# Performance work log

Hardware: AMD Instinct MI355X
Metric: run time of the kernel (lower is better)

The kernel has to match this reference:

```python
import jax, jax.numpy as jnp
import numpy as np

N_STREAMS = 4
SINKHORN_ITERS = 20
EPS = 1e-8


def sinkhorn_knopp(log_mat, num_iters=SINKHORN_ITERS, eps=EPS):
    mat = jnp.exp(log_mat)
    def body(_, m):
        m = m / (m.sum(axis=-2, keepdims=True) + eps)
        m = m / (m.sum(axis=-1, keepdims=True) + eps)
        return m
    return jax.lax.fori_loop(0, num_iters, body, mat)


def setup_inputs() -> dict:
    key = jax.random.key(0)
    B, L, C = 4, 2048, 1024
    n = N_STREAMS
    hidden = 4 * C
    ks = jax.random.split(key, 8)
    def xavier(k, shape):
        fan_in, fan_out = shape[0], shape[1]
        lim = np.sqrt(6.0 / (fan_in + fan_out))
        return jax.random.uniform(k, shape, jnp.float32, -lim, lim)
    return {
        "x": jax.random.normal(ks[0], (B, L, C), jnp.float32),
        "rms_weight": jnp.ones((C * n,), jnp.float32),
        "W_dyn": xavier(ks[1], (C * n, n * n + 2 * n)),  # Linear no-bias, stored [in,out]
        "bias_pre": jnp.zeros((1, n), jnp.float32),
        "bias_post": jnp.zeros((1, n), jnp.float32),
        "bias_res": jnp.zeros((n, n), jnp.float32),
        "alpha_pre": jnp.full((1,), 0.01, jnp.float32),
        "alpha_post": jnp.full((1,), 0.01, jnp.float32),
        "alpha_res": jnp.full((1,), 0.01, jnp.float32),
        "W1": xavier(ks[2], (C, hidden)),
        "b1": jnp.zeros((hidden,), jnp.float32),
        "W2": xavier(ks[3], (hidden, C)),
        "b2": jnp.zeros((C,), jnp.float32),
        "Wout": xavier(ks[4], (C * n, C)),
        "bout": jnp.zeros((C,), jnp.float32),
    }


def reference(x, rms_weight, W_dyn, bias_pre, bias_post, bias_res,
              alpha_pre, alpha_post, alpha_res, W1, b1, W2, b2, Wout, bout):
    B, L, C = x.shape
    n = bias_pre.shape[1]
    # x expanded across streams (broadcast view, no copy)
    x_exp = jnp.broadcast_to(x[:, :, None, :], (B, L, n, C))  # [B,L,n,C]
    x_flat = x_exp.reshape(B, L, n * C)
    # RMSNorm
    rms = jnp.sqrt(jnp.mean(x_flat * x_flat, axis=-1, keepdims=True) + EPS)
    x_norm = x_flat / rms * rms_weight
    # dynamic projection
    dynamic = x_norm @ W_dyn  # [B,L,n*n+2n]
    dyn_pre = dynamic[..., :n]
    dyn_post = dynamic[..., n:2 * n]
    dyn_res = dynamic[..., 2 * n:].reshape(B, L, n, n)
    H_pre = jax.nn.sigmoid(alpha_pre * dyn_pre + bias_pre)            # [B,L,n]
    H_post = 2.0 * jax.nn.sigmoid(alpha_post * dyn_post + bias_post)  # [B,L,n]
    H_res = sinkhorn_knopp(alpha_res * dyn_res + bias_res)            # [B,L,n,n]
    # pre-mix streams then residual MLP
    pre_mixed = jnp.einsum('bln,blnc->blc', H_pre, x_exp)
    h = jax.nn.gelu(pre_mixed @ W1 + b1, approximate=False)
    f_out = h @ W2 + b2  # [B,L,C]
    # post mixing + doubly-stochastic residual mixing
    post_mixed = H_post[..., None] * f_out[:, :, None, :]             # [B,L,n,C]
    res_mixed = jnp.einsum('blnm,blmc->blnc', H_res, x_exp)
    merged = (res_mixed + post_mixed).reshape(B, L, n * C)
    return merged @ Wout + bout + x
```

## Files before the change

### kernel.cpp

```cpp
#include <hip/hip_runtime.h>

typedef unsigned short u16;
typedef __bf16 bf16x8 __attribute__((ext_vector_type(8)));
typedef float f32x4 __attribute__((ext_vector_type(4)));

__device__ __forceinline__ u16 f2bf(float f) {
  unsigned int u = __builtin_bit_cast(unsigned int, f);
  u += 0x7fffu + ((u >> 16) & 1u);
  return (u16)(u >> 16);
}

__device__ __forceinline__ void gload_lds16(const u16* g, u16* l) {
  __builtin_amdgcn_global_load_lds((const __attribute__((address_space(1))) unsigned int*)g,
                                   (__attribute__((address_space(3))) unsigned int*)l,
                                   16, 0, 0);
}

__device__ __forceinline__ float gelu_erf(float v) {
  const float z = v * 0.70710678118654752f;
  const float az = fabsf(z);
  const float t = __builtin_amdgcn_rcpf(1.0f + 0.3275911f * az);
  const float p = t * (0.254829592f +
                  t * (-0.284496736f +
                  t * (1.421413741f +
                  t * (-1.453152027f + t * 1.061405429f))));
  const float e = __expf(-az * az);
  float er = 1.0f - p * e;
  er = (z < 0.f) ? -er : er;
  return 0.5f * v * (1.0f + er);
}


__global__ __launch_bounds__(256) void weff_kernel(const float* __restrict__ rmsw,
                                                   const float* __restrict__ Wdyn,
                                                   float* __restrict__ WT) {
  int idx = blockIdx.x * 256 + threadIdx.x;
  int j = idx >> 10, c = idx & 1023;
  float s = 0.f;
#pragma unroll
  for (int st = 0; st < 4; ++st) {
    int r = st * 1024 + c;
    s += rmsw[r] * Wdyn[(long)r * 24 + j];
  }
  WT[idx] = s;
}

__global__ __launch_bounds__(256) void pack_all(const float* __restrict__ W1,
                                                const float* __restrict__ W2,
                                                const float* __restrict__ WO,
                                                u16* __restrict__ F1,
                                                u16* __restrict__ F2,
                                                u16* __restrict__ FO) {
  const int blk = blockIdx.x;
  const int sel = blk >> 11;
  const float* W;
  u16* FMB;
  int lgN, KC;
  if (sel == 0)      { W = W1; FMB = F1; lgN = 12; KC = 32; }
  else if (sel == 1) { W = W2; FMB = F2; lgN = 10; KC = 128; }
  else               { W = WO; FMB = FO; lgN = 10; KC = 128; }
  const long gid = (long)(blk & 2047) * 256 + threadIdx.x;
  const int N = 1 << lgN;
  const int n = (int)(gid & (N - 1));
  const int k0 = (int)(gid >> lgN) * 8;
  unsigned int p[4];
#pragma unroll
  for (int d = 0; d < 4; ++d) {
    const float lo = W[(long)(k0 + 2 * d) * N + n];
    const float hi = W[(long)(k0 + 2 * d + 1) * N + n];
    p[d] = (unsigned)f2bf(lo) | ((unsigned)f2bf(hi) << 16);
  }
  const long ad = ((long)(n >> 4) * KC + (k0 >> 5)) * 512 +
                  ((n & 15) + (((k0 >> 3) & 3) << 4)) * 8;
  *(uint4*)(FMB + ad) = make_uint4(p[0], p[1], p[2], p[3]);
}

__global__ __launch_bounds__(512) void prep_tokens(
    const float* __restrict__ x, const float* __restrict__ WT,
    const float* __restrict__ bias_pre, const float* __restrict__ bias_post,
    const float* __restrict__ bias_res, const float* __restrict__ a_pre,
    const float* __restrict__ a_post, const float* __restrict__ a_res,
    u16* __restrict__ preA, float* __restrict__ scal) {
  const int tid = threadIdx.x;
  const int b = blockIdx.x;
  const long t0 = (long)b * 16;

  __shared__ float red[32][16][26];
  __shared__ float tot2[16][26];
  __shared__ float spre[16];

  {
    const int tt = tid & 15;
    const int cc = tid >> 4;
    const float* xp = x + (t0 + tt) * 1024 + cc * 32;
    float part[25];
#pragma unroll
    for (int j = 0; j < 25; ++j) part[j] = 0.f;
#pragma unroll
    for (int g = 0; g < 8; ++g) {
      const float4 xv = *(const float4*)(xp + g * 4);
      part[24] += xv.x * xv.x + xv.y * xv.y + xv.z * xv.z + xv.w * xv.w;
#pragma unroll
      for (int j = 0; j < 24; ++j) {
        const float4 wv = *(const float4*)(WT + (long)j * 1024 + cc * 32 + g * 4);
        part[j] += xv.x * wv.x + xv.y * wv.y + xv.z * wv.z + xv.w * wv.w;
      }
    }
#pragma unroll
    for (int j = 0; j < 25; ++j) red[cc][tt][j] = part[j];
  }
  __syncthreads();

  {
    const int tt = tid >> 5;
    const int j = tid & 31;
    if (j < 25) {
      float s = 0.f;
#pragma unroll
      for (int cc = 0; cc < 32; ++cc) s += red[cc][tt][j];
      tot2[tt][j] = s;
    }
  }
  __syncthreads();

  if (tid < 256) {
    const int tt = tid >> 4;
    const int m = tid & 15;
    const long t = t0 + tt;
    const float rms = sqrtf(tot2[tt][24] * (1.0f / 1024.0f) + 1e-8f);
    const float rinv = 1.0f / rms;

    if (m == 0) {
      const float ap = a_pre[0];
      float s_pre = 0.f;
#pragma unroll
      for (int i = 0; i < 4; ++i)
        s_pre += 1.f / (1.f + expf(-(ap * tot2[tt][i] * rinv + bias_pre[i])));
      spre[tt] = s_pre;
    }
    if (m < 4) {
      const float apo = a_post[0];
      float hp = 2.f / (1.f + expf(-(apo * tot2[tt][4 + m] * rinv + bias_post[m])));
      scal[t * 8 + 4 + m] = hp;
    }
    const float ar = a_res[0];
    float Mv = expf(ar * tot2[tt][8 + m] * rinv + bias_res[m]);
#pragma unroll
    for (int it = 0; it < 20; ++it) {
      float cs = Mv + __shfl_xor(Mv, 4);
      cs += __shfl_xor(cs, 8);
      Mv = Mv / (cs + 1e-8f);
      float rs = Mv + __shfl_xor(Mv, 1);
      rs += __shfl_xor(rs, 2);
      Mv = Mv / (rs + 1e-8f);
    }
    float rs = Mv + __shfl_xor(Mv, 1);
    rs += __shfl_xor(rs, 2);
    if ((m & 3) == 0) scal[t * 8 + (m >> 2)] = rs;
  }
  __syncthreads();

  {
    const int w = tid >> 6;
    const int lane = tid & 63;
    const int tl = lane & 15;
    const int co = (lane >> 4) * 8;
    const float sp = spre[tl];
#pragma unroll
    for (int p = 0; p < 4; ++p) {
      const int ki = p * 8 + w;
      const float* xr = x + (t0 + tl) * 1024 + ki * 32 + co;
      const float4 xa = *(const float4*)(xr);
      const float4 xb = *(const float4*)(xr + 4);
      unsigned q0 = (unsigned)f2bf(sp * xa.x) | ((unsigned)f2bf(sp * xa.y) << 16);
      unsigned q1 = (unsigned)f2bf(sp * xa.z) | ((unsigned)f2bf(sp * xa.w) << 16);
      unsigned q2 = (unsigned)f2bf(sp * xb.x) | ((unsigned)f2bf(sp * xb.y) << 16);
      unsigned q3 = (unsigned)f2bf(sp * xb.z) | ((unsigned)f2bf(sp * xb.w) << 16);
      *(uint4*)(preA + ((long)b * 32 + ki) * 512 + lane * 8) = make_uint4(q0, q1, q2, q3);
    }
  }
}

template <int EPI>
__global__ __launch_bounds__(256, 4) void gemm_fm(const u16* __restrict__ A,
                                                  const u16* __restrict__ B,
                                                  const int KCtot, const int GX,
                                                  const int N, const int KCout,
                                                  const float* __restrict__ bias,
                                                  const float* __restrict__ X,
                                                  const float* __restrict__ scal,
                                                  void* __restrict__ dstv) {
  const int tid = threadIdx.x;
  const int lane = tid & 63;
  const int wave = tid >> 6;
  const int wm = wave >> 1, wn = wave & 1;
  const int b = blockIdx.x;
  const int c = b & 7;
  const int s = b >> 3;
  const int bx = s % GX;
  const int by = c * 8 + s / GX;

  __shared__ u16 lds[2][16][512];

  const u16* gb[4];
  u16* lc[4];
#pragma unroll
  for (int l = 0; l < 4; ++l) {
    const int t = wave * 4 + l;
    gb[l] = (t < 8) ? (A + (long)(by * 8 + t) * KCtot * 512 + lane * 8)
                    : (B + (long)(bx * 8 + (t - 8)) * KCtot * 512 + lane * 8);
    lc[l] = &lds[0][t][0];
  }

#define STAGE(buf, kt)                                             \
  {                                                                \
    const long ko = (long)(kt)*512;                                \
    _Pragma("unroll") for (int l = 0; l < 4; ++l)                  \
        gload_lds16(gb[l] + ko, lc[l] + (buf)*8192);               \
  }

  f32x4 acc[4][4] = {};

  STAGE(0, 0);
  __syncthreads();

  for (int kt = 0; kt < KCtot; ++kt) {
    const int cur = kt & 1;
    if (kt + 1 < KCtot) STAGE(cur ^ 1, kt + 1);
    bf16x8 af[4], bfr[4];
#pragma unroll
    for (int i = 0; i < 4; ++i) {
      af[i] = *(const bf16x8*)&lds[cur][wm * 4 + i][lane * 8];
      bfr[i] = *(const bf16x8*)&lds[cur][8 + wn * 4 + i][lane * 8];
    }
#pragma unroll
    for (int i = 0; i < 4; ++i)
#pragma unroll
      for (int j = 0; j < 4; ++j)
        acc[i][j] = __builtin_amdgcn_mfma_f32_16x16x32_bf16(af[i], bfr[j], acc[i][j], 0, 0, 0);
    __syncthreads();
  }
#undef STAGE

  u16* ep = ((u16*)lds) + wave * 4096;

  if constexpr (EPI == 0) {
    u16* dst = (u16*)dstv;
#pragma unroll
    for (int i = 0; i < 4; ++i)
#pragma unroll
      for (int j = 0; j < 4; ++j) {
        const int col = bx * 128 + wn * 64 + j * 16 + (lane & 15);
        const float bcol = bias[col];
#pragma unroll
        for (int r = 0; r < 4; ++r) {
          const float g = gelu_erf(acc[i][j][r] + bcol);
          const int lp = ((lane >> 4) * 4 + r) | ((((j & 1) << 1) | ((lane & 15) >> 3)) << 4);
          ep[(i * 2 + (j >> 1)) * 512 + lp * 8 + (lane & 7)] = f2bf(g);
        }
      }
    __syncthreads();
#pragma unroll
    for (int ch = 0; ch < 8; ++ch) {
      const int i = ch >> 1, jc = ch & 1;
      const long row16 = by * 8 + wm * 4 + i;
      const long col32 = bx * 4 + wn * 2 + jc;
      *(uint4*)(dst + (row16 * KCout + col32) * 512 + lane * 8) =
          *(const uint4*)(ep + ch * 512 + lane * 8);
    }
  } else if constexpr (EPI == 1) {
    u16* dst = (u16*)dstv;
#pragma unroll
    for (int i = 0; i < 4; ++i) {
      float rr[4][4], hh[4][4];
#pragma unroll
      for (int r = 0; r < 4; ++r) {
        const int row = by * 128 + wm * 64 + i * 16 + (lane >> 4) * 4 + r;
        const float4 rv = *(const float4*)(scal + (long)row * 8);
        const float4 hv = *(const float4*)(scal + (long)row * 8 + 4);
        rr[r][0] = rv.x; rr[r][1] = rv.y; rr[r][2] = rv.z; rr[r][3] = rv.w;
        hh[r][0] = hv.x; hh[r][1] = hv.y; hh[r][2] = hv.z; hh[r][3] = hv.w;
      }
#pragma unroll
      for (int jc = 0; jc < 2; ++jc) {
        __syncthreads();
#pragma unroll
        for (int jj = 0; jj < 2; ++jj) {
          const int j = jc * 2 + jj;
          const int col = bx * 128 + wn * 64 + j * 16 + (lane & 15);
          const float bcol = bias[col];
#pragma unroll
          for (int r = 0; r < 4; ++r) {
            const int row = by * 128 + wm * 64 + i * 16 + (lane >> 4) * 4 + r;
            const float f = acc[i][j][r] + bcol;
            const float xval = X[(long)row * 1024 + col];
            const int lp = ((lane >> 4) * 4 + r) | (((jj << 1) | ((lane & 15) >> 3)) << 4);
#pragma unroll
            for (int ss = 0; ss < 4; ++ss)
              ep[ss * 512 + lp * 8 + (lane & 7)] = f2bf(rr[r][ss] * xval + hh[r][ss] * f);
          }
        }
        __syncthreads();
        const long row16 = by * 8 + wm * 4 + i;
        const long col32 = bx * 4 + wn * 2 + jc;
#pragma unroll
        for (int ss = 0; ss < 4; ++ss)
          *(uint4*)(dst + (row16 * 128 + (long)ss * 32 + col32) * 512 + lane * 8) =
              *(const uint4*)(ep + ss * 512 + lane * 8);
      }
    }
  } else {
    float* dst = (float*)dstv;
    float* ep32 = (float*)ep;
#pragma unroll
    for (int half = 0; half < 2; ++half) {
      __syncthreads();
#pragma unroll
      for (int i2 = 0; i2 < 2; ++i2) {
        const int i = half * 2 + i2;
#pragma unroll
        for (int j = 0; j < 4; ++j) {
          const int col = bx * 128 + wn * 64 + j * 16 + (lane & 15);
          const float bcol = bias[col];
#pragma unroll
          for (int r = 0; r < 4; ++r) {
            const long row = by * 128 + wm * 64 + i * 16 + (lane >> 4) * 4 + r;
            ep32[(i2 * 16 + (lane >> 4) * 4 + r) * 64 + j * 16 + (lane & 15)] =
                acc[i][j][r] + bcol + X[row * 1024 + col];
          }
        }
      }
      __syncthreads();
#pragma unroll
      for (int q = 0; q < 8; ++q) {
        const int lr = q * 4 + (lane >> 4);
        const long row = by * 128 + wm * 64 + half * 32 + lr;
        const long col = bx * 128 + wn * 64 + (lane & 15) * 4;
        *(float4*)(dst + row * 1024 + col) =
            *(const float4*)(ep32 + lr * 64 + (lane & 15) * 4);
      }
    }
  }
}

extern "C" void kernel_launch(void* const* d_in, const int* in_sizes, int n_in,
                              void* d_out, int out_size, void* d_ws, size_t ws_size,
                              hipStream_t stream) {
  (void)in_sizes; (void)n_in; (void)out_size; (void)ws_size;
  const float* x = (const float*)d_in[0];
  const float* rmsw = (const float*)d_in[1];
  const float* Wdyn = (const float*)d_in[2];
  const float* bias_pre = (const float*)d_in[3];
  const float* bias_post = (const float*)d_in[4];
  const float* bias_res = (const float*)d_in[5];
  const float* a_pre = (const float*)d_in[6];
  const float* a_post = (const float*)d_in[7];
  const float* a_res = (const float*)d_in[8];
  const float* W1 = (const float*)d_in[9];
  const float* b1 = (const float*)d_in[10];
  const float* W2 = (const float*)d_in[11];
  const float* b2 = (const float*)d_in[12];
  const float* Wout = (const float*)d_in[13];
  const float* bout = (const float*)d_in[14];
  float* out = (float*)d_out;
  char* ws = (char*)d_ws;

  constexpr size_t MB = 1048576;
  u16* W1fm = (u16*)(ws);
  u16* W2fm = (u16*)(ws + 8 * MB);
  u16* WOfm = (u16*)(ws + 16 * MB);
  float* WT = (float*)(ws + 24 * MB);
  float* scal = (float*)(ws + 24 * MB + 98304);
  u16* h = (u16*)(ws + 25 * MB);
  u16* merged = (u16*)(ws + 89 * MB);
  u16* preA = (u16*)(ws + 89 * MB);

  weff_kernel<<<96, 256, 0, stream>>>(rmsw, Wdyn, WT);
  pack_all<<<6144, 256, 0, stream>>>(W1, W2, Wout, W1fm, W2fm, WOfm);
  prep_tokens<<<512, 512, 0, stream>>>(x, WT, bias_pre, bias_post, bias_res,
                                       a_pre, a_post, a_res, preA, scal);
  gemm_fm<0><<<2048, 256, 0, stream>>>(preA, W1fm, 32, 32, 4096, 128, b1, nullptr, nullptr, h);
  gemm_fm<1><<<512, 256, 0, stream>>>(h, W2fm, 128, 8, 1024, 128, b2, x, scal, merged);
  gemm_fm<2><<<512, 256, 0, stream>>>(merged, WOfm, 128, 8, 1024, 0, bout, x, nullptr, out);
}
```

Baseline: 431.1 us.

## Enlarge GEMM tiles to 512 threads with 4-stage LDS pipeline and manual waitcnts

```diff
diff --git a/kernel.cpp b/kernel.cpp
--- a/kernel.cpp
+++ b/kernel.cpp
@@ -181,76 +181,94 @@
   }
 }
 
-template <int EPI>
-__global__ __launch_bounds__(256, 4) void gemm_fm(const u16* __restrict__ A,
-                                                  const u16* __restrict__ B,
-                                                  const int KCtot, const int GX,
-                                                  const int N, const int KCout,
-                                                  const float* __restrict__ bias,
-                                                  const float* __restrict__ X,
-                                                  const float* __restrict__ scal,
-                                                  void* __restrict__ dstv) {
+template <int EPI, int NT, int LGGX>
+__global__ __launch_bounds__(512, 2) void gemm_fm2(const u16* __restrict__ A,
+                                                   const u16* __restrict__ B,
+                                                   const int KCtot, const int KCout,
+                                                   const float* __restrict__ bias,
+                                                   const float* __restrict__ X,
+                                                   const float* __restrict__ scal,
+                                                   void* __restrict__ dstv) {
+  constexpr int CH = 16 + NT;
+  constexpr int SC = CH / 8;
+  constexpr int AI = (NT == 16) ? 8 : 4;
   const int tid = threadIdx.x;
   const int lane = tid & 63;
   const int wave = tid >> 6;
-  const int wm = wave >> 1, wn = wave & 1;
+  const int wm = (NT == 16) ? (wave >> 2) : (wave >> 1);
+  const int wn = (NT == 16) ? (wave & 3) : (wave & 1);
   const int b = blockIdx.x;
   const int c = b & 7;
   const int s = b >> 3;
-  const int bx = s % GX;
-  const int by = c * 8 + s / GX;
-
-  __shared__ u16 lds[2][16][512];
+  const int bx = s & ((1 << LGGX) - 1);
+  const int by = c * 4 + (s >> LGGX);
+
+  __shared__ u16 lds[4][CH][512];
+  u16* const l0 = (u16*)lds;
 
   const u16* gb[4];
-  u16* lc[4];
-#pragma unroll
-  for (int l = 0; l < 4; ++l) {
-    const int t = wave * 4 + l;
-    gb[l] = (t < 8) ? (A + (long)(by * 8 + t) * KCtot * 512 + lane * 8)
-                    : (B + (long)(bx * 8 + (t - 8)) * KCtot * 512 + lane * 8);
-    lc[l] = &lds[0][t][0];
-  }
-
-#define STAGE(buf, kt)                                             \
-  {                                                                \
-    const long ko = (long)(kt)*512;                                \
-    _Pragma("unroll") for (int l = 0; l < 4; ++l)                  \
-        gload_lds16(gb[l] + ko, lc[l] + (buf)*8192);               \
-  }
-
-  f32x4 acc[4][4] = {};
-
-  STAGE(0, 0);
-  __syncthreads();
+#pragma unroll
+  for (int l = 0; l < SC; ++l) {
+    const int t = wave * SC + l;
+    gb[l] = (t < 16) ? (A + ((long)(by * 16 + t) * KCtot) * 512 + lane * 8)
+                     : (B + ((long)(bx * NT + (t - 16)) * KCtot) * 512 + lane * 8);
+  }
+
+#define STG(kt)                                                              \
+  {                                                                          \
+    u16* cb_ = l0 + (((kt) & 3) * CH + wave * SC) * 512;                     \
+    const long ko_ = (long)(kt)*512;                                         \
+    _Pragma("unroll") for (int l_ = 0; l_ < SC; ++l_)                        \
+        gload_lds16(gb[l_] + ko_, cb_ + l_ * 512);                           \
+  }
+
+  f32x4 acc[AI][4] = {};
+
+  STG(0); STG(1); STG(2);
+  if constexpr (SC == 4) asm volatile("s_waitcnt vmcnt(8)" ::: "memory");
+  else                   asm volatile("s_waitcnt vmcnt(6)" ::: "memory");
+  __builtin_amdgcn_s_barrier();
 
   for (int kt = 0; kt < KCtot; ++kt) {
-    const int cur = kt & 1;
-    if (kt + 1 < KCtot) STAGE(cur ^ 1, kt + 1);
-    bf16x8 af[4], bfr[4];
-#pragma unroll
-    for (int i = 0; i < 4; ++i) {
-      af[i] = *(const bf16x8*)&lds[cur][wm * 4 + i][lane * 8];
-      bfr[i] = *(const bf16x8*)&lds[cur][8 + wn * 4 + i][lane * 8];
-    }
-#pragma unroll
-    for (int i = 0; i < 4; ++i)
+    if (kt + 3 < KCtot) STG(kt + 3);
+    const u16* cb = l0 + (kt & 3) * (CH * 512);
+    bf16x8 af[AI], bf[4];
+#pragma unroll
+    for (int i = 0; i < AI; ++i)
+      af[i] = *(const bf16x8*)(cb + (wm * AI + i) * 512 + lane * 8);
+#pragma unroll
+    for (int j = 0; j < 4; ++j)
+      bf[j] = *(const bf16x8*)(cb + (16 + wn * 4 + j) * 512 + lane * 8);
+    asm volatile("s_waitcnt lgkmcnt(0)" ::: "memory");
+    __builtin_amdgcn_sched_barrier(0);
+    __builtin_amdgcn_s_setprio(1);
+#pragma unroll
+    for (int i = 0; i < AI; ++i)
 #pragma unroll
       for (int j = 0; j < 4; ++j)
-        acc[i][j] = __builtin_amdgcn_mfma_f32_16x16x32_bf16(af[i], bfr[j], acc[i][j], 0, 0, 0);
-    __syncthreads();
-  }
-#undef STAGE
-
-  u16* ep = ((u16*)lds) + wave * 4096;
+        acc[i][j] = __builtin_amdgcn_mfma_f32_16x16x32_bf16(af[i], bf[j], acc[i][j], 0, 0, 0);
+    __builtin_amdgcn_s_setprio(0);
+    if (kt + 4 <= KCtot) {
+      if constexpr (SC == 4) asm volatile("s_waitcnt vmcnt(8)" ::: "memory");
+      else                   asm volatile("s_waitcnt vmcnt(6)" ::: "memory");
+    } else if (kt + 3 == KCtot) {
+      if constexpr (SC == 4) asm volatile("s_waitcnt vmcnt(4)" ::: "memory");
+      else                   asm volatile("s_waitcnt vmcnt(3)" ::: "memory");
+    } else {
+      asm volatile("s_waitcnt vmcnt(0)" ::: "memory");
+    }
+    __builtin_amdgcn_s_barrier();
+  }
+#undef STG
 
   if constexpr (EPI == 0) {
     u16* dst = (u16*)dstv;
-#pragma unroll
-    for (int i = 0; i < 4; ++i)
+    u16* ep = l0 + wave * 8192;
+#pragma unroll
+    for (int i = 0; i < AI; ++i)
 #pragma unroll
       for (int j = 0; j < 4; ++j) {
-        const int col = bx * 128 + wn * 64 + j * 16 + (lane & 15);
+        const int col = bx * 256 + wn * 64 + j * 16 + (lane & 15);
         const float bcol = bias[col];
 #pragma unroll
         for (int r = 0; r < 4; ++r) {
@@ -259,23 +277,23 @@
           ep[(i * 2 + (j >> 1)) * 512 + lp * 8 + (lane & 7)] = f2bf(g);
         }
       }
-    __syncthreads();
-#pragma unroll
-    for (int ch = 0; ch < 8; ++ch) {
+#pragma unroll
+    for (int ch = 0; ch < 2 * AI; ++ch) {
       const int i = ch >> 1, jc = ch & 1;
-      const long row16 = by * 8 + wm * 4 + i;
-      const long col32 = bx * 4 + wn * 2 + jc;
+      const long row16 = by * 16 + wm * 8 + i;
+      const long col32 = bx * 8 + wn * 2 + jc;
       *(uint4*)(dst + (row16 * KCout + col32) * 512 + lane * 8) =
           *(const uint4*)(ep + ch * 512 + lane * 8);
     }
   } else if constexpr (EPI == 1) {
     u16* dst = (u16*)dstv;
-#pragma unroll
-    for (int i = 0; i < 4; ++i) {
+    u16* ep = l0 + wave * 4096;
+#pragma unroll
+    for (int i = 0; i < AI; ++i) {
       float rr[4][4], hh[4][4];
 #pragma unroll
       for (int r = 0; r < 4; ++r) {
-        const int row = by * 128 + wm * 64 + i * 16 + (lane >> 4) * 4 + r;
+        const int row = by * 256 + wm * 64 + i * 16 + (lane >> 4) * 4 + r;
         const float4 rv = *(const float4*)(scal + (long)row * 8);
         const float4 hv = *(const float4*)(scal + (long)row * 8 + 4);
         rr[r][0] = rv.x; rr[r][1] = rv.y; rr[r][2] = rv.z; rr[r][3] = rv.w;
@@ -283,7 +301,6 @@
       }
 #pragma unroll
       for (int jc = 0; jc < 2; ++jc) {
-        __syncthreads();
 #pragma unroll
         for (int jj = 0; jj < 2; ++jj) {
           const int j = jc * 2 + jj;
@@ -291,7 +308,7 @@
           const float bcol = bias[col];
 #pragma unroll
           for (int r = 0; r < 4; ++r) {
-            const int row = by * 128 + wm * 64 + i * 16 + (lane >> 4) * 4 + r;
+            const int row = by * 256 + wm * 64 + i * 16 + (lane >> 4) * 4 + r;
             const float f = acc[i][j][r] + bcol;
             const float xval = X[(long)row * 1024 + col];
             const int lp = ((lane >> 4) * 4 + r) | (((jj << 1) | ((lane & 15) >> 3)) << 4);
@@ -300,8 +317,7 @@
               ep[ss * 512 + lp * 8 + (lane & 7)] = f2bf(rr[r][ss] * xval + hh[r][ss] * f);
           }
         }
-        __syncthreads();
-        const long row16 = by * 8 + wm * 4 + i;
+        const long row16 = by * 16 + wm * 4 + i;
         const long col32 = bx * 4 + wn * 2 + jc;
 #pragma unroll
         for (int ss = 0; ss < 4; ++ss)
@@ -311,10 +327,9 @@
     }
   } else {
     float* dst = (float*)dstv;
-    float* ep32 = (float*)ep;
+    float* ep32 = (float*)(l0 + wave * 4096);
 #pragma unroll
     for (int half = 0; half < 2; ++half) {
-      __syncthreads();
 #pragma unroll
       for (int i2 = 0; i2 < 2; ++i2) {
         const int i = half * 2 + i2;
@@ -324,17 +339,16 @@
           const float bcol = bias[col];
 #pragma unroll
           for (int r = 0; r < 4; ++r) {
-            const long row = by * 128 + wm * 64 + i * 16 + (lane >> 4) * 4 + r;
+            const long row = by * 256 + wm * 64 + i * 16 + (lane >> 4) * 4 + r;
             ep32[(i2 * 16 + (lane >> 4) * 4 + r) * 64 + j * 16 + (lane & 15)] =
                 acc[i][j][r] + bcol + X[row * 1024 + col];
           }
         }
       }
-      __syncthreads();
 #pragma unroll
       for (int q = 0; q < 8; ++q) {
         const int lr = q * 4 + (lane >> 4);
-        const long row = by * 128 + wm * 64 + half * 32 + lr;
+        const long row = by * 256 + wm * 64 + half * 32 + lr;
         const long col = bx * 128 + wn * 64 + (lane & 15) * 4;
         *(float4*)(dst + row * 1024 + col) =
             *(const float4*)(ep32 + lr * 64 + (lane & 15) * 4);
@@ -379,7 +393,7 @@
   pack_all<<<6144, 256, 0, stream>>>(W1, W2, Wout, W1fm, W2fm, WOfm);
   prep_tokens<<<512, 512, 0, stream>>>(x, WT, bias_pre, bias_post, bias_res,
                                        a_pre, a_post, a_res, preA, scal);
-  gemm_fm<0><<<2048, 256, 0, stream>>>(preA, W1fm, 32, 32, 4096, 128, b1, nullptr, nullptr, h);
-  gemm_fm<1><<<512, 256, 0, stream>>>(h, W2fm, 128, 8, 1024, 128, b2, x, scal, merged);
-  gemm_fm<2><<<512, 256, 0, stream>>>(merged, WOfm, 128, 8, 1024, 0, bout, x, nullptr, out);
-}
+  gemm_fm2<0, 16, 4><<<512, 512, 0, stream>>>(preA, W1fm, 32, 128, b1, nullptr, nullptr, h);
+  gemm_fm2<1, 8, 3><<<256, 512, 0, stream>>>(h, W2fm, 128, 128, b2, x, scal, merged);
+  gemm_fm2<2, 8, 3><<<256, 512, 0, stream>>>(merged, WOfm, 128, 0, bout, x, nullptr, out);
+}
```

Result: faster. 420.5 us (-2.5%).
